# Optimization experiments

Measured on AMD Instinct MI355X. Metric: run time of the kernel, lower is better.

Reference implementation:

```python
import jax, jax.numpy as jnp
import numpy as np

B, L, H, N2, NLAYERS = 8, 4096, 256, 32, 4


def setup_inputs() -> dict:
    key = jax.random.key(0)
    ks = jax.random.split(key, 7)
    x = jax.random.normal(ks[0], (B, L, H), dtype=jnp.float32)
    # S4D kernel params (per layer, stacked on leading dim)
    dt_min, dt_max = 1e-3, 1e-1
    u = jax.random.uniform(ks[1], (NLAYERS, H), dtype=jnp.float32)
    log_dt = u * (np.log(dt_max) - np.log(dt_min)) + np.log(dt_min)
    log_A_real = jnp.log(0.5 * jnp.ones((NLAYERS, H, N2), jnp.float32))
    A_imag = jnp.broadcast_to(np.pi * jnp.arange(N2, dtype=jnp.float32), (NLAYERS, H, N2)) * jnp.ones((NLAYERS, H, N2), jnp.float32)
    C_re = jax.random.normal(ks[2], (NLAYERS, H, N2), dtype=jnp.float32) * (0.5 ** 0.5)
    C_im = jax.random.normal(ks[3], (NLAYERS, H, N2), dtype=jnp.float32) * (0.5 ** 0.5)
    D = jax.random.normal(ks[4], (NLAYERS, H), dtype=jnp.float32)
    Wout = jax.random.normal(ks[5], (NLAYERS, 2 * H, H), dtype=jnp.float32) * (1.0 / H) ** 0.5
    bout = jnp.zeros((NLAYERS, 2 * H), jnp.float32)
    ln_g = jnp.ones((NLAYERS, H), jnp.float32)
    ln_b = jnp.zeros((NLAYERS, H), jnp.float32)
    return dict(x=x, log_dt=log_dt, log_A_real=log_A_real, A_imag=A_imag,
                C_re=C_re, C_im=C_im, D=D, Wout=Wout, bout=bout,
                ln_g=ln_g, ln_b=ln_b)


def _s4d_kernel(log_dt, log_A_real, A_imag, C_re, C_im, Lseq):
    # Vandermonde kernel of S4D: k[h,l] = 2*Re sum_n C'_hn exp(dt_h*A_hn*l)
    dt = jnp.exp(log_dt)                       # (H,)
    A = (-jnp.exp(log_A_real) + 1j * A_imag)   # (H,N) complex
    C = C_re + 1j * C_im                       # (H,N)
    dtA = A * dt[:, None]                      # (H,N)
    K = jnp.exp(dtA[:, :, None] * jnp.arange(Lseq, dtype=jnp.float32))  # (H,N,L)
    Cm = C * (jnp.exp(dtA) - 1.0) / A          # ZOH discretization of C
    return 2.0 * jnp.einsum('hn,hnl->hl', Cm, K).real  # (H,L)


def _s4d_layer(u, log_dt, log_A_real, A_imag, C_re, C_im, D, Wout, bout):
    # u: (B,H,L)
    Lq = u.shape[-1]
    k = _s4d_kernel(log_dt, log_A_real, A_imag, C_re, C_im, Lq)  # (H,L)
    kf = jnp.fft.rfft(k, n=2 * Lq)             # (H, L+1)
    uf = jnp.fft.rfft(u, n=2 * Lq)             # (B,H,L+1)
    y = jnp.fft.irfft(uf * kf, n=2 * Lq)[..., :Lq]
    y = y + u * D[:, None]
    y = jax.nn.gelu(y, approximate=False)
    # output linear: 1x1 conv H->2H followed by GLU along channel dim
    y = jnp.einsum('oh,bhl->bol', Wout, y) + bout[None, :, None]
    a, b = jnp.split(y, 2, axis=1)
    return a * jax.nn.sigmoid(b)               # (B,H,L)


def _layernorm_ch(x, g, b, eps=1e-5):
    # x: (B,H,L); normalize over channel axis H (matches norm on (B,L,H))
    m = jnp.mean(x, axis=1, keepdims=True)
    v = jnp.mean((x - m) ** 2, axis=1, keepdims=True)
    return (x - m) / jnp.sqrt(v + eps) * g[None, :, None] + b[None, :, None]


def reference(x, log_dt, log_A_real, A_imag, C_re, C_im, D, Wout, bout, ln_g, ln_b):
    u = jnp.swapaxes(x, -1, -2)  # (B,H,L)
    for i in range(NLAYERS):  # post-norm (prenorm=False), dropout=identity (eval)
        z = _s4d_layer(u, log_dt[i], log_A_real[i], A_imag[i], C_re[i], C_im[i],
                       D[i], Wout[i], bout[i])
        u = z + u
        u = _layernorm_ch(u, ln_g[i], ln_b[i])
    return jnp.swapaxes(u, -1, -2)  # (B,L,H)
```

## Files before the change

kernel.cpp:

```cpp
#include <hip/hip_runtime.h>
#include <math.h>

#define B    8
#define L    4096
#define H    256
#define N2   32
#define NL   4
#define O2   512
#define BLK  64
#define NBLK 64
#define TVP  136
#define MJP  72
#define UTP  72
#define INP  68
#define TL2  64
#define YPAD 264
#define URP  72

typedef __attribute__((ext_vector_type(8))) short short8;
typedef __attribute__((ext_vector_type(4))) float f32x4;

__device__ __forceinline__ unsigned short f2bf(float f)
{
    unsigned int u = __float_as_uint(f);
    unsigned int r = (u + 0x7fffu + ((u >> 16) & 1u)) >> 16;
    return (unsigned short)r;
}

__device__ __forceinline__ float bf2f(unsigned short v)
{
    return __uint_as_float(((unsigned int)v) << 16);
}

__device__ __forceinline__ float gelu_f(float x)
{
    float t = 1.59576912161f * fmaf(0.044715f * x * x, x, x);
    return x / (1.f + __expf(-t));
}

__global__ __launch_bounds__(256) void k_setup(
    const float* __restrict__ x, const float* __restrict__ log_dt,
    const float* __restrict__ log_Ar, const float* __restrict__ A_im,
    const float* __restrict__ C_re, const float* __restrict__ C_im,
    const float* __restrict__ Dv, const float* __restrict__ Wout,
    unsigned short* __restrict__ Wb, unsigned short* __restrict__ TVc,
    unsigned short* __restrict__ Mm, float2* __restrict__ w64c,
    unsigned short* __restrict__ u)
{
    __shared__ float sh[32 * 68];
    const int bid = blockIdx.x;
    const int t = threadIdx.x;

    if (bid < 512) {
        int idx = (bid * 256 + t) * 4;
        float4 v = *(const float4*)(Wout + idx);
        ushort4 o;
        o.x = f2bf(v.x); o.y = f2bf(v.y); o.z = f2bf(v.z); o.w = f2bf(v.w);
        *(ushort4*)(Wb + idx) = o;
    } else if (bid < 640) {
        float* kb = sh;
        const int g = t >> 5, n = t & 31;
        const int id = (bid - 512) * 8 + g;
        const int layer = id >> 8, h = id & 255;
        const int idx = (layer * H + h) * N2 + n;
        double dt = exp((double)log_dt[layer * H + h]);
        double Ar = -exp((double)log_Ar[idx]);
        double Ai = (double)A_im[idx];
        double dtr = dt * Ar, dti = dt * Ai;
        double er = exp(dtr);
        double dwr = er * cos(dti), dwi = er * sin(dti);
        double numr = dwr - 1.0, numi = dwi;
        double den = Ar * Ar + Ai * Ai;
        double qr0 = (numr * Ar + numi * Ai) / den;
        double qi0 = (numi * Ar - numr * Ai) / den;
        double dcr = (double)C_re[idx], dci = (double)C_im[idx];
        const float wr = (float)dwr, wi = (float)dwi;
        const float cr = (float)(2.0 * (dcr * qr0 - dci * qi0));
        const float ci = (float)(2.0 * (dcr * qi0 + dci * qr0));
        const float Dh = Dv[layer * H + h];
        unsigned short* tv = TVc + (size_t)(layer * H + h) * BLK * TVP;
        unsigned short* mm = Mm + (size_t)(layer * H + h) * BLK * MJP;
        float vr = 1.f, vi = 0.f;
        for (int d = 0; d < BLK; ++d) {
            float pk = fmaf(cr, vr, -(ci * vi));
            pk += __shfl_xor(pk, 1);  pk += __shfl_xor(pk, 2);
            pk += __shfl_xor(pk, 4);  pk += __shfl_xor(pk, 8);
            pk += __shfl_xor(pk, 16);
            if (n == 0) kb[g * 64 + d] = pk;
            mm[n * MJP + (63 - d)]        = f2bf(vr);
            mm[(32 + n) * MJP + (63 - d)] = f2bf(vi);
            float nvr = vr * wr - vi * wi;
            float nvi = vr * wi + vi * wr;
            vr = nvr; vi = nvi;
            float qr = fmaf(cr, vr, -(ci * vi));
            float qi = fmaf(cr, vi, ci * vr);
            tv[d * TVP + 64 + n] = f2bf(qr);
            tv[d * TVP + 96 + n] = f2bf(-qi);
        }
        w64c[(layer * H + h) * N2 + n] = make_float2(vr, vi);
        __syncthreads();
        for (int i = 0; i < BLK; ++i) {
#pragma unroll
            for (int hf = 0; hf < 2; ++hf) {
                int j = n + hf * 32;
                float val = (j > i) ? 0.f : ((j == i) ? (kb[g * 64] + Dh) : kb[g * 64 + i - j]);
                tv[i * TVP + j] = f2bf(val);
            }
        }
    } else {
        const int rb = bid - 640;
        const int hx = rb & 7, ly = (rb >> 3) & 63, b = rb >> 9;
        const int h0 = hx * 32, l0 = ly * 64;
        const int tx = t & 7, ty = t >> 3;
        const float* xb = x + ((size_t)b * L + l0) * H + h0;
#pragma unroll
        for (int i = 0; i < 2; ++i) {
            int l = ty + i * 32;
            float4 v = *(const float4*)(xb + (size_t)l * H + tx * 4);
            sh[(tx * 4 + 0) * 68 + l] = v.x;
            sh[(tx * 4 + 1) * 68 + l] = v.y;
            sh[(tx * 4 + 2) * 68 + l] = v.z;
            sh[(tx * 4 + 3) * 68 + l] = v.w;
        }
        __syncthreads();
        const int hh = t >> 3, cc = (t & 7) * 8;
        const float* row = &sh[hh * 68 + cc];
        short8 o8;
#pragma unroll
        for (int j = 0; j < 8; ++j) o8[j] = (short)f2bf(row[j]);
        *(short8*)(u + ((size_t)b * H + h0 + hh) * L + l0 + cc) = o8;
    }
}

__global__ __launch_bounds__(256) void k_scan3(
    const unsigned short* __restrict__ u, const unsigned short* __restrict__ Mm_l,
    const unsigned short* __restrict__ TVc_l, const float2* __restrict__ w64c_l,
    unsigned short* __restrict__ y)
{
    __shared__ __align__(16) unsigned short uT[BLK * UTP];
    __shared__ __align__(16) unsigned short ST[BLK * UTP];
    __shared__ __align__(16) float INC[BLK * INP];
    __shared__ float2 cLd[4][32];
    const int t = threadIdx.x;
    const int wv = t >> 6, lane = t & 63;
    const int lanei = lane & 15, quad = lane >> 4;
    const int h = blockIdx.x >> 3, ct = blockIdx.x & 7;
    const unsigned short* ub = u + (size_t)(ct * H + h) * L;

    const unsigned short* arowA = Mm_l + (size_t)h * BLK * MJP + (wv * 16 + lanei) * MJP + quad * 8;
    short8 mA[2];
    mA[0] = *(const short8*)(arowA);
    mA[1] = *(const short8*)(arowA + 32);
    const unsigned short* arowB = TVc_l + (size_t)h * BLK * TVP + (wv * 16 + lanei) * TVP + quad * 8;
    short8 tB[4];
#pragma unroll
    for (int kt = 0; kt < 4; ++kt)
        tB[kt] = *(const short8*)(arowB + kt * 32);
    const float2 w64 = w64c_l[h * N2 + (lane & 31)];

    {
        int col = t >> 2, q = t & 3;
        *(short8*)&uT[col * UTP + q * 16]     = *(const short8*)(ub + col * 64 + q * 16);
        *(short8*)&uT[col * UTP + q * 16 + 8] = *(const short8*)(ub + col * 64 + q * 16 + 8);
    }
    __syncthreads();

    {
        f32x4 acc[4];
#pragma unroll
        for (int nt = 0; nt < 4; ++nt) acc[nt] = (f32x4){0.f, 0.f, 0.f, 0.f};
#pragma unroll
        for (int kt = 0; kt < 2; ++kt) {
#pragma unroll
            for (int nt = 0; nt < 4; ++nt) {
                short8 b8 = *(const short8*)&uT[(nt * 16 + lanei) * UTP + kt * 32 + quad * 8];
                acc[nt] = __builtin_amdgcn_mfma_f32_16x16x32_bf16(mA[kt], b8, acc[nt], 0, 0, 0);
            }
        }
#pragma unroll
        for (int nt = 0; nt < 4; ++nt)
            *(f32x4*)&INC[(nt * 16 + lanei) * INP + wv * 16 + quad * 4] = acc[nt];
    }
    __syncthreads();

    const int n = lane & 31;
    float Pr[16], Pi[16];
    float w1r = 1.f, w1i = 0.f;
    if (lane < 32) {
        float sr = 0.f, si = 0.f;
        const int base = wv * 16;
#pragma unroll
        for (int k = 0; k < 16; ++k) {
            Pr[k] = sr; Pi[k] = si;
            float ir = INC[(base + k) * INP + n];
            float ii = INC[(base + k) * INP + 32 + n];
            float nr = fmaf(w64.x, sr, fmaf(-w64.y, si, ir));
            float ni = fmaf(w64.x, si, fmaf(w64.y, sr, ii));
            sr = nr; si = ni;
        }
        cLd[wv][n] = make_float2(sr, si);
        float ar = w64.x, ai = w64.y;
#pragma unroll
        for (int q = 0; q < 4; ++q) {
            float nr2 = ar * ar - ai * ai;
            float ni2 = 2.f * ar * ai;
            ar = nr2; ai = ni2;
        }
        w1r = ar; w1i = ai;
    }
    __syncthreads();
    if (lane < 32) {
        float Cr = 0.f, Ci = 0.f;
        for (int wp = 0; wp < wv; ++wp) {
            float2 Lw = cLd[wp][n];
            float nr = fmaf(w1r, Cr, fmaf(-w1i, Ci, Lw.x));
            float ni = fmaf(w1r, Ci, fmaf(w1i, Cr, Lw.y));
            Cr = nr; Ci = ni;
        }
        float pr = 1.f, pi = 0.f;
#pragma unroll
        for (int k = 0; k < 16; ++k) {
            int blk = wv * 16 + k;
            float Sr = fmaf(pr, Cr, fmaf(-pi, Ci, Pr[k]));
            float Si = fmaf(pr, Ci, fmaf(pi, Cr, Pi[k]));
            ST[blk * UTP + n]      = f2bf(Sr);
            ST[blk * UTP + 32 + n] = f2bf(Si);
            float npr = pr * w64.x - pi * w64.y;
            float npi = pr * w64.y + pi * w64.x;
            pr = npr; pi = npi;
        }
    }
    __syncthreads();

    {
        f32x4 acc[4];
#pragma unroll
        for (int nt = 0; nt < 4; ++nt) acc[nt] = (f32x4){0.f, 0.f, 0.f, 0.f};
#pragma unroll
        for (int kt = 0; kt < 4; ++kt) {
            const unsigned short* bb = (kt < 2) ? uT : ST;
            int ko = (kt & 1) * 32 + quad * 8;
#pragma unroll
            for (int nt = 0; nt < 4; ++nt) {
                short8 b8 = *(const short8*)&bb[(nt * 16 + lanei) * UTP + ko];
                acc[nt] = __builtin_amdgcn_mfma_f32_16x16x32_bf16(tB[kt], b8, acc[nt], 0, 0, 0);
            }
        }
        unsigned short* yb = y + (size_t)(ct * H + h) * L;
#pragma unroll
        for (int nt = 0; nt < 4; ++nt) {
            int blk = nt * 16 + lanei;
            int i0 = wv * 16 + quad * 4;
            ushort4 o4;
            o4.x = f2bf(gelu_f(acc[nt][0]));
            o4.y = f2bf(gelu_f(acc[nt][1]));
            o4.z = f2bf(gelu_f(acc[nt][2]));
            o4.w = f2bf(gelu_f(acc[nt][3]));
            *(ushort4*)(yb + blk * 64 + i0) = o4;
        }
    }
}

__global__ __launch_bounds__(512, 4) void k_gemm(
    const unsigned short* __restrict__ y, unsigned short* __restrict__ u,
    const unsigned short* __restrict__ Wb, const float* __restrict__ bo,
    const float* __restrict__ lng, const float* __restrict__ lnb,
    float* __restrict__ outp)
{
    __shared__ __align__(16) unsigned short yS[H * URP];
    __shared__ float bS[O2];
    __shared__ float lgS[H], lbS[H];
    __shared__ float redS[8][4][16], redQ[8][4][16];

    const int t = threadIdx.x;
    const int wv = t >> 6;
    const int lane = t & 63;
    const int lanei = lane & 15;
    const int quad = lane >> 4;
    const int b = blockIdx.x >> 6;
    const int l0 = (blockIdx.x & 63) * TL2;

    size_t abase[2][2];
#pragma unroll
    for (int p = 0; p < 2; ++p)
#pragma unroll
        for (int jj = 0; jj < 2; ++jj)
            abase[p][jj] = (size_t)(p * 256 + wv * 32 + jj * 16 + lanei) * H + quad * 8;

    short8 a8p[4];
#pragma unroll
    for (int p = 0; p < 2; ++p)
#pragma unroll
        for (int jj = 0; jj < 2; ++jj)
            a8p[p * 2 + jj] = *(const short8*)(Wb + abase[p][jj]);

    {
        const int i = t & 7, hr = t >> 3;
        const unsigned short* yb = y + (size_t)b * H * L + l0 + i * 8;
#pragma unroll
        for (int ps = 0; ps < 4; ++ps) {
            int h = ps * 64 + hr;
            short8 v8 = *(const short8*)(yb + (size_t)h * L);
#pragma unroll
            for (int r = 0; r < 8; ++r)
                yS[(i * 8 + r) * YPAD + (h ^ (8 * i))] = (unsigned short)v8[r];
        }
        if (t < O2) bS[t] = bo[t];
        if (t < H) { lgS[t] = lng[t]; lbS[t] = lnb[t]; }
    }
    __syncthreads();

    f32x4 acc[2][2][4];
#pragma unroll
    for (int p = 0; p < 2; ++p)
#pragma unroll
        for (int jj = 0; jj < 2; ++jj)
#pragma unroll
            for (int nt = 0; nt < 4; ++nt)
                acc[p][jj][nt] = (f32x4){0.f, 0.f, 0.f, 0.f};

#pragma unroll
    for (int kt = 0; kt < 8; ++kt) {
        short8 bfr[4];
#pragma unroll
        for (int nt = 0; nt < 4; ++nt) {
            int lp = nt * 16 + lanei;
            int a = (2 * nt + (lanei >> 3)) & 7;
            bfr[nt] = *(const short8*)&yS[lp * YPAD + ((kt * 32 + quad * 8) ^ (8 * a))];
        }
#pragma unroll
        for (int p = 0; p < 2; ++p)
#pragma unroll
            for (int jj = 0; jj < 2; ++jj) {
                short8 a8 = (kt == 0) ? a8p[p * 2 + jj]
                                      : *(const short8*)(Wb + abase[p][jj] + kt * 32);
#pragma unroll
                for (int nt = 0; nt < 4; ++nt)
                    acc[p][jj][nt] = __builtin_amdgcn_mfma_f32_16x16x32_bf16(
                        a8, bfr[nt], acc[p][jj][nt], 0, 0, 0);
            }
    }
    __syncthreads();

    unsigned short* ub = u + (size_t)b * H * L + l0;
#pragma unroll
    for (int r = 0; r < 4; ++r) {
        int c = r * 512 + t;
        int o = c >> 3, c8 = (c & 7) * 8;
        *(short8*)&yS[o * URP + c8] = *(const short8*)(ub + (size_t)o * L + c8);
    }
    __syncthreads();

    float psum[4] = {0.f, 0.f, 0.f, 0.f}, psq[4] = {0.f, 0.f, 0.f, 0.f};
#pragma unroll
    for (int jj = 0; jj < 2; ++jj) {
#pragma unroll
        for (int nt = 0; nt < 4; ++nt) {
            int lc = nt * 16 + lanei;
#pragma unroll
            for (int reg = 0; reg < 4; ++reg) {
                int o = wv * 32 + jj * 16 + quad * 4 + reg;
                float a = acc[0][jj][nt][reg] + bS[o];
                float g = acc[1][jj][nt][reg] + bS[o + 256];
                float glu = a / (1.f + __expf(-g));
                float val = glu + bf2f(yS[o * URP + lc]);
                acc[0][jj][nt][reg] = val;
                psum[nt] += val;
                psq[nt] = fmaf(val, val, psq[nt]);
            }
        }
    }
#pragma unroll
    for (int nt = 0; nt < 4; ++nt) {
        psum[nt] += __shfl_xor(psum[nt], 16);
        psum[nt] += __shfl_xor(psum[nt], 32);
        psq[nt]  += __shfl_xor(psq[nt], 16);
        psq[nt]  += __shfl_xor(psq[nt], 32);
    }
    if (lane < 16) {
#pragma unroll
        for (int nt = 0; nt < 4; ++nt) {
            redS[wv][nt][lanei] = psum[nt];
            redQ[wv][nt][lanei] = psq[nt];
        }
    }
    __syncthreads();
    float mcol[4], icol[4];
#pragma unroll
    for (int nt = 0; nt < 4; ++nt) {
        float s = 0.f, q = 0.f;
#pragma unroll
        for (int w = 0; w < 8; ++w) { s += redS[w][nt][lanei]; q += redQ[w][nt][lanei]; }
        float m = s * (1.0f / 256.0f);
        float v = q * (1.0f / 256.0f) - m * m;
        mcol[nt] = m;
        icol[nt] = rsqrtf(v + 1e-5f);
    }
    if (outp == nullptr) {
#pragma unroll
        for (int jj = 0; jj < 2; ++jj) {
#pragma unroll
            for (int nt = 0; nt < 4; ++nt) {
                int lc = nt * 16 + lanei;
#pragma unroll
                for (int reg = 0; reg < 4; ++reg) {
                    int o = wv * 32 + jj * 16 + quad * 4 + reg;
                    float val = acc[0][jj][nt][reg];
                    float ov = (val - mcol[nt]) * icol[nt] * lgS[o] + lbS[o];
                    yS[o * URP + lc] = f2bf(ov);
                }
            }
        }
        __syncthreads();
#pragma unroll
        for (int r = 0; r < 4; ++r) {
            int c = r * 512 + t;
            int o = c >> 3, c8 = (c & 7) * 8;
            *(short8*)(ub + (size_t)o * L + c8) = *(const short8*)&yS[o * URP + c8];
        }
    } else {
#pragma unroll
        for (int jj = 0; jj < 2; ++jj) {
#pragma unroll
            for (int nt = 0; nt < 4; ++nt) {
                int lc = nt * 16 + lanei;
                int o0 = wv * 32 + jj * 16 + quad * 4;
                float4 ov;
#pragma unroll
                for (int reg = 0; reg < 4; ++reg) {
                    int o = o0 + reg;
                    float val = acc[0][jj][nt][reg];
                    ((float*)&ov)[reg] = (val - mcol[nt]) * icol[nt] * lgS[o] + lbS[o];
                }
                *(float4*)(outp + ((size_t)b * L + l0 + lc) * H + o0) = ov;
            }
        }
    }
}

extern "C" void kernel_launch(void* const* d_in, const int* in_sizes, int n_in,
                              void* d_out, int out_size, void* d_ws, size_t ws_size,
                              hipStream_t stream)
{
    const float* x      = (const float*)d_in[0];
    const float* log_dt = (const float*)d_in[1];
    const float* log_Ar = (const float*)d_in[2];
    const float* A_im   = (const float*)d_in[3];
    const float* C_re   = (const float*)d_in[4];
    const float* C_im   = (const float*)d_in[5];
    const float* Dv     = (const float*)d_in[6];
    const float* Wout   = (const float*)d_in[7];
    const float* bout   = (const float*)d_in[8];
    const float* lng    = (const float*)d_in[9];
    const float* lnb    = (const float*)d_in[10];
    float* out = (float*)d_out;

    unsigned short* u   = (unsigned short*)d_ws;
    unsigned short* Wb  = u + (size_t)B * H * L;
    unsigned short* TVc = Wb + (size_t)NL * O2 * H;
    unsigned short* Mm  = TVc + (size_t)NL * H * BLK * TVP;
    float2* w64c        = (float2*)(Mm + (size_t)NL * H * BLK * MJP);
    unsigned short* y   = (unsigned short*)(w64c + (size_t)NL * H * N2);

    k_setup<<<4736, 256, 0, stream>>>(x, log_dt, log_Ar, A_im, C_re, C_im, Dv, Wout,
                                      Wb, TVc, Mm, w64c, u);
    for (int layer = 0; layer < NL; ++layer) {
        k_scan3<<<H * 8, 256, 0, stream>>>(u, Mm + (size_t)layer * H * BLK * MJP,
                                           TVc + (size_t)layer * H * BLK * TVP,
                                           w64c + (size_t)layer * H * N2, y);
        k_gemm<<<B * L / TL2, 512, 0, stream>>>(y, u, Wb + (size_t)layer * O2 * H,
                                                bout + layer * O2, lng + layer * H, lnb + layer * H,
                                                (layer == NL - 1) ? out : nullptr);
    }
}
```

Measured before the change: 323.5 us.

## Parallelize S4D kernel setup with closed-form powers and staged coalesced stores

The setup kernel now uses one block per (layer, channel) instead of one warp. Each power of the discretized pole is computed directly from magnitude and phase (exp/sincos) rather than by a serial 64-step complex recurrence. The Toeplitz and Vandermonde tiles are built in shared memory and written out to global memory with 16-byte vector stores, replacing the earlier strided scalar writes. The fast-math __expf/__cosf/__sinf calls may differ slightly in precision from the recurrence, and shared memory per block grows.

```diff
diff --git a/kernel.cpp b/kernel.cpp
--- a/kernel.cpp
+++ b/kernel.cpp
@@ -47,7 +47,7 @@
     unsigned short* __restrict__ Mm, float2* __restrict__ w64c,
     unsigned short* __restrict__ u)
 {
-    __shared__ float sh[32 * 68];
+    __shared__ __align__(16) unsigned char smem_raw[27648];
     const int bid = blockIdx.x;
     const int t = threadIdx.x;
 
@@ -57,58 +57,88 @@
         ushort4 o;
         o.x = f2bf(v.x); o.y = f2bf(v.y); o.z = f2bf(v.z); o.w = f2bf(v.w);
         *(ushort4*)(Wb + idx) = o;
-    } else if (bid < 640) {
-        float* kb = sh;
-        const int g = t >> 5, n = t & 31;
-        const int id = (bid - 512) * 8 + g;
+    } else if (bid < 1536) {
+        unsigned short* tvS = (unsigned short*)smem_raw;
+        unsigned short* mmS = tvS + BLK * TVP;
+        float* kbS = (float*)(mmS + BLK * MJP);
+        float* cS  = kbS + BLK;
+        const int id = bid - 512;
         const int layer = id >> 8, h = id & 255;
-        const int idx = (layer * H + h) * N2 + n;
-        double dt = exp((double)log_dt[layer * H + h]);
-        double Ar = -exp((double)log_Ar[idx]);
-        double Ai = (double)A_im[idx];
-        double dtr = dt * Ar, dti = dt * Ai;
-        double er = exp(dtr);
-        double dwr = er * cos(dti), dwi = er * sin(dti);
-        double numr = dwr - 1.0, numi = dwi;
-        double den = Ar * Ar + Ai * Ai;
-        double qr0 = (numr * Ar + numi * Ai) / den;
-        double qi0 = (numi * Ar - numr * Ai) / den;
-        double dcr = (double)C_re[idx], dci = (double)C_im[idx];
-        const float wr = (float)dwr, wi = (float)dwi;
-        const float cr = (float)(2.0 * (dcr * qr0 - dci * qi0));
-        const float ci = (float)(2.0 * (dcr * qi0 + dci * qr0));
-        const float Dh = Dv[layer * H + h];
-        unsigned short* tv = TVc + (size_t)(layer * H + h) * BLK * TVP;
-        unsigned short* mm = Mm + (size_t)(layer * H + h) * BLK * MJP;
-        float vr = 1.f, vi = 0.f;
-        for (int d = 0; d < BLK; ++d) {
+        if (t < 32) {
+            const int n0 = t;
+            const int idx = (layer * H + h) * N2 + n0;
+            double dt = exp((double)log_dt[layer * H + h]);
+            double Ar = -exp((double)log_Ar[idx]);
+            double Ai = (double)A_im[idx];
+            double dtr = dt * Ar, dti = dt * Ai;
+            double er = exp(dtr);
+            double dwr = er * cos(dti), dwi = er * sin(dti);
+            double numr = dwr - 1.0, numi = dwi;
+            double den = Ar * Ar + Ai * Ai;
+            double qr0 = (numr * Ar + numi * Ai) / den;
+            double qi0 = (numi * Ar - numr * Ai) / den;
+            double dcr = (double)C_re[idx], dci = (double)C_im[idx];
+            cS[n0]       = (float)(2.0 * (dcr * qr0 - dci * qi0));
+            cS[32 + n0]  = (float)(2.0 * (dcr * qi0 + dci * qr0));
+            cS[64 + n0]  = (float)dwr;
+            cS[96 + n0]  = (float)dwi;
+            double rev = dti * 0.15915494309189535;
+            cS[128 + n0] = (float)(rev - floor(rev));
+            cS[160 + n0] = (float)dtr;
+            double m64 = exp(64.0 * dtr);
+            double a64 = 64.0 * dti;
+            w64c[(layer * H + h) * N2 + n0] =
+                make_float2((float)(m64 * cos(a64)), (float)(m64 * sin(a64)));
+        }
+        __syncthreads();
+        const int n = t & 31, dg = t >> 5;
+        const float cr = cS[n], ci = cS[32 + n];
+        const float wr = cS[64 + n], wi = cS[96 + n];
+        const float revf = cS[128 + n], dtrf = cS[160 + n];
+#pragma unroll
+        for (int i = 0; i < 8; ++i) {
+            const int d = dg * 8 + i;
+            float ph = (float)d * revf;
+            ph = (ph - floorf(ph)) * 6.28318530718f;
+            float mag = __expf((float)d * dtrf);
+            float vr = mag * __cosf(ph);
+            float vi = mag * __sinf(ph);
             float pk = fmaf(cr, vr, -(ci * vi));
             pk += __shfl_xor(pk, 1);  pk += __shfl_xor(pk, 2);
             pk += __shfl_xor(pk, 4);  pk += __shfl_xor(pk, 8);
             pk += __shfl_xor(pk, 16);
-            if (n == 0) kb[g * 64 + d] = pk;
-            mm[n * MJP + (63 - d)]        = f2bf(vr);
-            mm[(32 + n) * MJP + (63 - d)] = f2bf(vi);
-            float nvr = vr * wr - vi * wi;
-            float nvi = vr * wi + vi * wr;
-            vr = nvr; vi = nvi;
-            float qr = fmaf(cr, vr, -(ci * vi));
-            float qi = fmaf(cr, vi, ci * vr);
-            tv[d * TVP + 64 + n] = f2bf(qr);
-            tv[d * TVP + 96 + n] = f2bf(-qi);
-        }
-        w64c[(layer * H + h) * N2 + n] = make_float2(vr, vi);
+            if (n == 0) kbS[d] = pk;
+            mmS[n * MJP + (63 - d)]        = f2bf(vr);
+            mmS[(32 + n) * MJP + (63 - d)] = f2bf(vi);
+            float v1r = vr * wr - vi * wi;
+            float v1i = vr * wi + vi * wr;
+            tvS[d * TVP + 64 + n] = f2bf(fmaf(cr, v1r, -(ci * v1i)));
+            tvS[d * TVP + 96 + n] = f2bf(-fmaf(cr, v1i, ci * v1r));
+        }
         __syncthreads();
-        for (int i = 0; i < BLK; ++i) {
-#pragma unroll
-            for (int hf = 0; hf < 2; ++hf) {
-                int j = n + hf * 32;
-                float val = (j > i) ? 0.f : ((j == i) ? (kb[g * 64] + Dh) : kb[g * 64 + i - j]);
-                tv[i * TVP + j] = f2bf(val);
-            }
-        }
+        {
+            const int r = t >> 2, c0 = (t & 3) * 16;
+            const float diag = kbS[0] + Dv[layer * H + h];
+            short8 o8[2];
+#pragma unroll
+            for (int j = 0; j < 16; ++j) {
+                int c = c0 + j;
+                float val = (c > r) ? 0.f : ((c == r) ? diag : kbS[r - c]);
+                o8[j >> 3][j & 7] = (short)f2bf(val);
+            }
+            *(short8*)&tvS[r * TVP + c0]     = o8[0];
+            *(short8*)&tvS[r * TVP + c0 + 8] = o8[1];
+        }
+        __syncthreads();
+        unsigned short* tv = TVc + (size_t)(layer * H + h) * BLK * TVP;
+        unsigned short* mm = Mm + (size_t)(layer * H + h) * BLK * MJP;
+        for (int c = t; c < (BLK * TVP) / 8; c += 256)
+            *(short8*)(tv + c * 8) = *(const short8*)&tvS[c * 8];
+        for (int c = t; c < (BLK * MJP) / 8; c += 256)
+            *(short8*)(mm + c * 8) = *(const short8*)&mmS[c * 8];
     } else {
-        const int rb = bid - 640;
+        float* sh = (float*)smem_raw;
+        const int rb = bid - 1536;
         const int hx = rb & 7, ly = (rb >> 3) & 63, b = rb >> 9;
         const int h0 = hx * 32, l0 = ly * 64;
         const int tx = t & 7, ty = t >> 3;
@@ -462,7 +492,7 @@
     float2* w64c        = (float2*)(Mm + (size_t)NL * H * BLK * MJP);
     unsigned short* y   = (unsigned short*)(w64c + (size_t)NL * H * N2);
 
-    k_setup<<<4736, 256, 0, stream>>>(x, log_dt, log_Ar, A_im, C_re, C_im, Dv, Wout,
+    k_setup<<<5632, 256, 0, stream>>>(x, log_dt, log_Ar, A_im, C_re, C_im, Dv, Wout,
                                       Wb, TVc, Mm, w64c, u);
     for (int layer = 0; layer < NL; ++layer) {
         k_scan3<<<H * 8, 256, 0, stream>>>(u, Mm + (size_t)layer * H * BLK * MJP,
```

Result: faster. 298.9 us (-7.6%).
